# Optimization experiments

Hardware: AMD Instinct MI355X
Metric: run time of the kernel (lower is better)

Reference implementation:

```python
import jax, jax.numpy as jnp
import numpy as np

DIM = 384
HEADS = 12
K = 3          # kernel_size
PAD = 1
STRIDE = 1
B, H, W = 8, 56, 56


def conv1x1(x, w, b=None):
    # x: [B,C,H,W], w: [O,C]
    y = jnp.einsum('bchw,oc->bohw', x, w)
    if b is not None:
        y = y + b[None, :, None, None]
    return y


def unfold(x, k, p, s):
    # torch nn.Unfold: returns patches [B, C, k*k, nH, nW], kernel row-major, channel-major overall
    Bx, C, Hx, Wx = x.shape
    nH = (Hx + 2 * p - k) // s + 1
    nW = (Wx + 2 * p - k) // s + 1
    xp = jnp.pad(x, ((0, 0), (0, 0), (p, p), (p, p)))
    cols = [xp[:, :, i:i + s * nH:s, j:j + s * nW:s] for i in range(k) for j in range(k)]
    return jnp.stack(cols, axis=2), nH, nW


def fold(col, Hx, Wx, k, p, s):
    # torch F.fold (col2im): scatter-add overlapping windows. col: [B, C, k*k, nH, nW]
    Bx, C, _, nH, nW = col.shape
    canvas = jnp.zeros((Bx, C, Hx + 2 * p, Wx + 2 * p), col.dtype)
    idx = 0
    for i in range(k):
        for j in range(k):
            canvas = canvas.at[:, :, i:i + s * nH:s, j:j + s * nW:s].add(col[:, :, idx])
            idx += 1
    return canvas[:, :, p:p + Hx, p:p + Wx]


def setup_inputs() -> dict:
    key = jax.random.key(0)
    ks = jax.random.split(key, 5)
    k2 = K * K
    x = jax.random.normal(ks[0], (B, DIM, H, W), dtype=jnp.float32)
    v_w = jax.random.normal(ks[1], (DIM, DIM), dtype=jnp.float32) * 0.02
    v_b = jnp.zeros((DIM,), dtype=jnp.float32)
    attn_w = jax.random.normal(ks[2], (k2 * k2 * HEADS, DIM), dtype=jnp.float32) * 0.02
    proj_w = jax.random.normal(ks[3], (DIM, DIM), dtype=jnp.float32) * 0.02
    return {'x': x, 'v_w': v_w, 'v_b': v_b, 'attn_w': attn_w, 'proj_w': proj_w}


def reference(x, v_w, v_b, attn_w, proj_w):
    Bx, C, Hx, Wx = x.shape
    k2 = K * K
    hd = C // HEADS  # head dim
    # value projection + unfold into overlapping k x k windows
    v = conv1x1(x, v_w, v_b)
    vcol, nH, nW = unfold(v, K, PAD, STRIDE)        # [B, C, k2, nH, nW]
    L = nH * nW
    v = vcol.reshape(Bx, HEADS, hd, k2, L)          # split C = (heads, hd), heads slow
    v = v.transpose(0, 1, 4, 3, 2)                  # [B, n, L, k2(d), hd]
    # adaptive avg pool to (nH, nW); with stride=1 this is identity (pool window 1)
    ph, pw = Hx // nH, Wx // nW
    xp = x.reshape(Bx, C, nH, ph, nW, pw).mean(axis=(3, 5))
    # per-pixel attention logits, channel layout = ((i*k2 + d)*HEADS + head)
    a = jnp.einsum('bchw,oc->bohw', xp, attn_w)     # [B, k2*k2*n, nH, nW]
    a = a.reshape(Bx, k2, k2, HEADS, L)             # [B, i, d, n, L]
    a = a.transpose(0, 3, 4, 1, 2)                  # [B, n, L, i, d]
    a = jax.nn.softmax(a, axis=-1)
    out = jnp.einsum('bnlid,bnldh->bnlih', a, v)    # [B, n, L, i, hd]
    out = out.transpose(0, 1, 4, 3, 2)              # [B, n, hd, i, L] -> channel (n*hd+h)
    out = out.reshape(Bx, C, k2, nH, nW)
    out = fold(out, Hx, Wx, K, PAD, STRIDE)         # scatter-add windows back
    return conv1x1(out, proj_w)
```

## Files before the change

### kernel.cpp

```cpp
#include <hip/hip_runtime.h>
#include <hip/hip_bf16.h>

#define DIM   384
#define HEADS 12
#define K2    9
#define HH    56
#define WW    56
#define HWP   3136
#define BB    8
#define AO    972
#define AOP   976
#define MCAT  1408
#define PP    3200
#define PPAD  3600
#define W60   60

#define WBLK     2688
#define HALOBLK  696

typedef __hip_bfloat16 bf16;
typedef short bf16x8 __attribute__((ext_vector_type(8)));
typedef short bf16x4v __attribute__((ext_vector_type(4)));
typedef float f32x4 __attribute__((ext_vector_type(4)));
typedef float f32x2 __attribute__((ext_vector_type(2)));

static __device__ __forceinline__ float b2f(bf16 v) { return __bfloat162float(v); }
static __device__ __forceinline__ float bs2f(short s) {
    return __uint_as_float(((unsigned int)(unsigned short)s) << 16);
}
static __device__ __forceinline__ short f2bs(float f) {
    __hip_bfloat16 h = __float2bfloat16(f);
    return *(short*)&h;
}
static __device__ __forceinline__ f32x2 unpk(unsigned int u) {
    f32x2 r;
    r[0] = __uint_as_float(u << 16);
    r[1] = __uint_as_float(u & 0xffff0000u);
    return r;
}

static __device__ __forceinline__ void gl_lds16(const bf16* g, bf16* l) {
    __builtin_amdgcn_global_load_lds(
        (const __attribute__((address_space(1))) unsigned int*)g,
        (__attribute__((address_space(3))) unsigned int*)l, 16, 0, 0);
}

__global__ __launch_bounds__(256) void prep_kernel(
        const float* __restrict__ x, const float* __restrict__ v_w,
        const float* __restrict__ attn_w, const float* __restrict__ proj_w,
        bf16* __restrict__ xT, bf16* __restrict__ wcat, bf16* __restrict__ wp,
        bf16* __restrict__ vP) {
    const int bid = blockIdx.x;
    if (bid < 400) {
        const int lane = threadIdx.x & 63, w = threadIdx.x >> 6;
        const int p = (bid % 50) * 64 + lane;
        const int b = bid / 50;
        bf16* dst = xT + ((size_t)b * PP + p) * DIM;
        if (p >= HWP) {
            bf16x8 z = {};
            for (int cg = w; cg < 48; cg += 4) *(bf16x8*)(dst + cg * 8) = z;
            return;
        }
        const float* src = x + (size_t)b * DIM * HWP + p;
        for (int cg = w; cg < 48; cg += 4) {
            bf16x8 v;
#pragma unroll
            for (int j = 0; j < 8; j++) v[j] = f2bs(src[(size_t)(cg * 8 + j) * HWP]);
            *(bf16x8*)(dst + cg * 8) = v;
        }
    } else if (bid < 400 + WBLK) {
        const int idx = (bid - 400) * 256 + threadIdx.x;
        const int NCAT = MCAT * DIM;
        if (idx < NCAT) {
            const int row = idx / DIM, col = idx % DIM;
            float v;
            if (row < 384) v = v_w[row * DIM + col];
            else { const int r2 = row - 384; v = (r2 < AO) ? attn_w[r2 * DIM + col] : 0.f; }
            *(short*)&wcat[idx] = f2bs(v);
        } else {
            const int j = idx - NCAT;
            if (j < 384 * DIM) *(short*)&wp[j] = f2bs(proj_w[j]);
        }
    } else {
        const int hidx = (bid - 400 - WBLK) * 256 + threadIdx.x;
        const int b = hidx / 22272;
        const int r = hidx % 22272;
        const int hp = r / 48, cgi = r % 48;
        int row, col;
        if (hp < 240) {
            const int rr = hp / 60;
            row = (rr < 2) ? rr : rr + 56;
            col = hp % 60;
        } else {
            const int h2 = hp - 240;
            row = 2 + (h2 >> 2);
            const int c4 = h2 & 3;
            col = (c4 < 2) ? c4 : c4 + 56;
        }
        bf16x8 z = {};
        *(bf16x8*)(vP + ((size_t)b * PPAD + row * W60 + col) * DIM + cgi * 8) = z;
    }
}

#define GEMM_STAGE(Ab, Bb, lA, lB, koff)                                       \
    {                                                                          \
        _Pragma("unroll")                                                      \
        for (int r = 0; r < 4; r++) {                                          \
            int idx = r * 256 + t;                                             \
            int row = idx >> 3;                                                \
            int kq = ((idx & 7) - (row >> 1)) & 7;                             \
            gl_lds16(Ab + (size_t)row * DIM + (koff) + kq * 8, lA + idx * 8);  \
        }                                                                      \
        _Pragma("unroll")                                                      \
        for (int r = 0; r < 4; r++) {                                          \
            int idx = r * 256 + t;                                             \
            int row = idx >> 3;                                                \
            int kq = ((idx & 7) - (row >> 1)) & 7;                             \
            gl_lds16(Bb + (size_t)row * DIM + (koff) + kq * 8, lB + idx * 8);  \
        }                                                                      \
    }

#define GEMM_COMPUTE(lA, lB, acc)                                              \
    __builtin_amdgcn_s_setprio(1);                                             \
    _Pragma("unroll")                                                          \
    for (int h = 0; h < 2; h++) {                                              \
        const int swzh = (((h << 2) + quad + (l16 >> 1)) & 7) * 8;             \
        bf16x8 af[4], bfr[4];                                                  \
        _Pragma("unroll")                                                      \
        for (int mt = 0; mt < 4; mt++)                                         \
            af[mt] = *(const bf16x8*)((lA) + (wm * 64 + mt * 16 + l16) * 64 + swzh); \
        _Pragma("unroll")                                                      \
        for (int nt = 0; nt < 4; nt++)                                         \
            bfr[nt] = *(const bf16x8*)((lB) + (wn * 64 + nt * 16 + l16) * 64 + swzh); \
        _Pragma("unroll")                                                      \
        for (int mt = 0; mt < 4; mt++)                                         \
            _Pragma("unroll")                                                  \
            for (int nt = 0; nt < 4; nt++)                                     \
                acc[mt][nt] = __builtin_amdgcn_mfma_f32_16x16x32_bf16(         \
                    af[mt], bfr[nt], acc[mt][nt], 0, 0, 0);                    \
    }                                                                          \
    __builtin_amdgcn_s_setprio(0);

#define GEMM_KSTEP(cA, cB, sA, sB, koff)                                       \
    GEMM_STAGE(Ab, Bb, sA, sB, koff)                                           \
    asm volatile("s_waitcnt vmcnt(8)" ::: "memory");                           \
    __builtin_amdgcn_s_barrier();                                              \
    GEMM_COMPUTE(cA, cB, acc)                                                  \
    asm volatile("s_waitcnt lgkmcnt(0)" ::: "memory");                         \
    __builtin_amdgcn_s_barrier();

#define GEMM_MAIN_LOOP_V6(Ab, Bb, acc)                                         \
    GEMM_STAGE(Ab, Bb, lA0, lB0, 0)                                            \
    GEMM_KSTEP(lA0, lB0, lA1, lB1, 64)                                         \
    GEMM_KSTEP(lA1, lB1, lA0, lB0, 128)                                        \
    GEMM_KSTEP(lA0, lB0, lA1, lB1, 192)                                        \
    GEMM_KSTEP(lA1, lB1, lA0, lB0, 256)                                        \
    GEMM_KSTEP(lA0, lB0, lA1, lB1, 320)                                        \
    asm volatile("s_waitcnt vmcnt(0)" ::: "memory");                           \
    __builtin_amdgcn_s_barrier();                                              \
    GEMM_COMPUTE(lA1, lB1, acc)

__global__ __launch_bounds__(256) void gemm12_kernel(
        const bf16* __restrict__ A, const bf16* __restrict__ Bt,
        const float* __restrict__ bias, bf16* __restrict__ vP,
        bf16* __restrict__ lT) {
    __shared__ bf16 lds[32768];
    bf16* lA0 = lds;
    bf16* lB0 = lds + 8192;
    bf16* lA1 = lds + 16384;
    bf16* lB1 = lds + 24576;
    const int t = threadIdx.x;
    const int lane = t & 63, w = t >> 6;
    const int wm = w & 1, wn = w >> 1;
    const int quad = lane >> 4, l16 = lane & 15;

    const int bid = blockIdx.x;
    const int swz = (bid & 7) * 275 + (bid >> 3);
    const int mtile = swz % 11;
    const int nb = swz / 11;
    const int ntile = nb % 25;
    const int b = nb / 25;
    const int n0 = ntile * 128;
    const int m0 = mtile * 128;

    const bf16* Ab = A + (size_t)m0 * DIM;
    const bf16* Bb = Bt + ((size_t)b * PP + n0) * DIM;

    f32x4 acc[4][4] = {};
    GEMM_MAIN_LOOP_V6(Ab, Bb, acc)

    const bool isv = (m0 < 384);
    const int ch0 = isv ? m0 : m0 - 384;

    bf16* wbuf = lds + w * 1152;
    const int nr = lane >> 2;
    const int mc = (lane & 3) * 16;
#pragma unroll
    for (int nt = 0; nt < 4; nt++) {
#pragma unroll
        for (int mt = 0; mt < 4; mt++) {
            float4 bi = make_float4(0.f, 0.f, 0.f, 0.f);
            if (isv) bi = *(const float4*)(bias + ch0 + wm * 64 + mt * 16 + quad * 4);
            bf16x4v pk;
            pk[0] = f2bs(acc[mt][nt][0] + bi.x);
            pk[1] = f2bs(acc[mt][nt][1] + bi.y);
            pk[2] = f2bs(acc[mt][nt][2] + bi.z);
            pk[3] = f2bs(acc[mt][nt][3] + bi.w);
            *(bf16x4v*)(wbuf + l16 * 72 + mt * 16 + quad * 4) = pk;
        }
        bf16x8 v0 = *(const bf16x8*)(wbuf + nr * 72 + mc);
        bf16x8 v1 = *(const bf16x8*)(wbuf + nr * 72 + mc + 8);
        const int p = n0 + wn * 64 + nt * 16 + nr;
        const int cc = ch0 + wm * 64 + mc;
        if (p < HWP && (isv || cc < AOP)) {
            bf16* dp;
            if (isv) {
                const int y = p / WW;
                dp = vP + ((size_t)b * PPAD + p + y * 4 + 122) * DIM + cc;
            } else {
                dp = lT + ((size_t)b * PP + p) * AOP + cc;
            }
            *(bf16x8*)dp = v0;
            *(bf16x8*)(dp + 8) = v1;
        }
    }
}

__global__ __launch_bounds__(256) void gemm_planar_kernel(
        const bf16* __restrict__ A, const bf16* __restrict__ Bt,
        float* __restrict__ out) {
    __shared__ bf16 lds[32768];
    bf16* lA0 = lds;
    bf16* lB0 = lds + 8192;
    bf16* lA1 = lds + 16384;
    bf16* lB1 = lds + 24576;
    const int t = threadIdx.x;
    const int lane = t & 63, w = t >> 6;
    const int wm = w & 1, wn = w >> 1;
    const int quad = lane >> 4, l16 = lane & 15;

    const int bid = blockIdx.x;
    const int swz = (bid & 7) * 75 + (bid >> 3);
    const int mtile = swz % 3;
    const int nb = swz / 3;
    const int ntile = nb % 25;
    const int b = nb / 25;
    const int n0 = ntile * 128;
    const int m0 = mtile * 128;

    const bf16* Ab = A + (size_t)m0 * DIM;
    const bf16* Bb = Bt + ((size_t)b * PP + n0) * DIM;

    f32x4 acc[4][4] = {};
    GEMM_MAIN_LOOP_V6(Ab, Bb, acc)

#pragma unroll
    for (int mt = 0; mt < 4; mt++) {
#pragma unroll
        for (int nt = 0; nt < 4; nt++) {
            int p = n0 + wn * 64 + nt * 16 + l16;
            if (p >= HWP) continue;
#pragma unroll
            for (int reg = 0; reg < 4; reg++) {
                int o = m0 + wm * 64 + mt * 16 + quad * 4 + reg;
                out[((size_t)b * DIM + o) * HWP + p] = acc[mt][nt][reg];
            }
        }
    }
}

__global__ __launch_bounds__(384) void attn_fold_kernel(
        const bf16* __restrict__ lT, const bf16* __restrict__ vP,
        bf16* __restrict__ cT) {
    __shared__ bf16 P[8 * 9 * 12 * 9];
    __shared__ float Wf[8 * 25 * 12];
    const int t = threadIdx.x;
    const int b = blockIdx.x & 7;
    const int pix0 = (blockIdx.x >> 3) * 8;
    const int Y = pix0 / WW, X0 = pix0 % WW;

    for (int r = t; r < 864; r += 384) {
        const int px = r / 108, rem = r % 108;
        const int i = rem / 12, n = rem % 12;
        const int ir = i / 3, ic = i % 3;
        const int yi = Y + 1 - ir, xi = X0 + px + 1 - ic;
        bf16* Pd = &P[r * 9];
        if (yi < 0 || yi >= HH || xi < 0 || xi >= WW) {
#pragma unroll
            for (int d = 0; d < K2; d++) *(short*)&Pd[d] = 0;
        } else {
            const bf16* base = lT + ((size_t)b * PP + yi * WW + xi) * AOP + i * 108 + n;
            float lv[K2];
            float m = -1e30f;
#pragma unroll
            for (int d = 0; d < K2; d++) {
                lv[d] = b2f(base[d * 12]);
                m = fmaxf(m, lv[d]);
            }
            float s = 0.f;
#pragma unroll
            for (int d = 0; d < K2; d++) { lv[d] = __expf(lv[d] - m); s += lv[d]; }
            const float inv = 1.f / s;
#pragma unroll
            for (int d = 0; d < K2; d++) *(short*)&Pd[d] = f2bs(lv[d] * inv);
        }
    }
    __syncthreads();

    if (t < 300) {
        const int off = t / 12, n = t % 12;
        const int dy = off / 5 - 2, dx = off % 5 - 2;
        const int ir_lo = max(0, -dy), ir_hi = min(2, 2 - dy);
        const int ic_lo = max(0, -dx), ic_hi = min(2, 2 - dx);
#pragma unroll
        for (int px = 0; px < 8; px++) {
            float wsum = 0.f;
            for (int ir = ir_lo; ir <= ir_hi; ir++)
                for (int ic = ic_lo; ic <= ic_hi; ic++) {
                    const int i = ir * 3 + ic;
                    const int d = (dy + ir) * 3 + (dx + ic);
                    wsum += b2f(P[((px * 9 + i) * 12 + n) * 9 + d]);
                }
            Wf[(px * 25 + off) * 12 + n] = wsum;
        }
    }
    __syncthreads();

    const int px = t / 48, cg = t % 48;
    const int X = X0 + px;
    const int n = cg >> 2;
    const float* Wp = &Wf[px * 300 + n];
    const bf16* vbp = vP + ((size_t)b * PPAD + (size_t)(Y + 2) * W60 + (X + 2)) * DIM + cg * 8;
    f32x2 a2[4] = {};
#pragma unroll
    for (int dy = -2; dy <= 2; dy++) {
        const bf16* rowb = vbp + dy * (W60 * DIM);
        const float* wrow = Wp + (dy + 2) * 60;
#pragma unroll
        for (int dx = -2; dx <= 2; dx++) {
            const float w = wrow[(dx + 2) * 12];
            const uint4 d = *(const uint4*)(rowb + dx * DIM);
            f32x2 w2; w2[0] = w; w2[1] = w;
            a2[0] = __builtin_elementwise_fma(unpk(d.x), w2, a2[0]);
            a2[1] = __builtin_elementwise_fma(unpk(d.y), w2, a2[1]);
            a2[2] = __builtin_elementwise_fma(unpk(d.z), w2, a2[2]);
            a2[3] = __builtin_elementwise_fma(unpk(d.w), w2, a2[3]);
        }
    }
    bf16x8 po;
#pragma unroll
    for (int j = 0; j < 4; j++) {
        po[2 * j]     = f2bs(a2[j][0]);
        po[2 * j + 1] = f2bs(a2[j][1]);
    }
    *(bf16x8*)(cT + ((size_t)b * PP + pix0 + px) * DIM + cg * 8) = po;
}

extern "C" void kernel_launch(void* const* d_in, const int* in_sizes, int n_in,
                              void* d_out, int out_size, void* d_ws, size_t ws_size,
                              hipStream_t stream) {
    const float* x      = (const float*)d_in[0];
    const float* v_w    = (const float*)d_in[1];
    const float* v_b    = (const float*)d_in[2];
    const float* attn_w = (const float*)d_in[3];
    const float* proj_w = (const float*)d_in[4];
    float* out = (float*)d_out;

    bf16* xT    = (bf16*)d_ws;
    bf16* vP    = xT + (size_t)BB * PP * DIM;
    bf16* lT    = vP + (size_t)BB * PPAD * DIM;
    bf16* wcat  = lT + (size_t)BB * PP * AOP;
    bf16* wp    = wcat + (size_t)MCAT * DIM;
    bf16* cT    = xT;

    const int nprep = 400 + WBLK + HALOBLK;
    prep_kernel<<<nprep, 256, 0, stream>>>(x, v_w, attn_w, proj_w, xT, wcat, wp, vP);

    gemm12_kernel<<<2200, 256, 0, stream>>>(wcat, xT, v_b, vP, lT);
    attn_fold_kernel<<<3136, 384, 0, stream>>>(lT, vP, cT);
    gemm_planar_kernel<<<600, 256, 0, stream>>>(wp, cT, out);
}
```

Baseline: 202.8 us.

## Keep B tile resident in LDS and loop over all M tiles per block

The fused value/logit GEMM now loads a 64-column slice of the activation matrix (full K=384) into LDS once per block. It then iterates over all 11 weight row-tiles, streaming A in double-buffered 64-wide K chunks. This removes repeated re-reads of the activation tile across M tiles and cuts the grid from 2200 to 400 blocks. The cost is larger LDS use, a smaller per-wave N tile, and fewer blocks to cover the GPU's 256 CUs.

```diff
diff --git a/kernel.cpp b/kernel.cpp
--- a/kernel.cpp
+++ b/kernel.cpp
@@ -160,68 +160,132 @@
     __builtin_amdgcn_s_barrier();                                              \
     GEMM_COMPUTE(lA1, lB1, acc)
 
+#define STAGE_A7(mi, kg, dst)                                                  \
+    { _Pragma("unroll")                                                        \
+      for (int r = 0; r < 4; r++) {                                            \
+          int idx = r * 256 + t;                                               \
+          int row = idx >> 3;                                                  \
+          int kq = ((idx & 7) - (row >> 1)) & 7;                               \
+          gl_lds16(A + (size_t)((mi) * 128 + row) * DIM + (kg) * 64 + kq * 8,  \
+                   dst + idx * 8);                                             \
+      } }
+
+#define COMPUTE7(lA, kg, acc)                                                  \
+    __builtin_amdgcn_s_setprio(1);                                             \
+    _Pragma("unroll")                                                          \
+    for (int h = 0; h < 2; h++) {                                              \
+        const int swzh = (((h << 2) + quad + (l16 >> 1)) & 7) * 8;             \
+        bf16x8 af[4], bfr[2];                                                  \
+        _Pragma("unroll")                                                      \
+        for (int mt = 0; mt < 4; mt++)                                         \
+            af[mt] = *(const bf16x8*)((lA) + (wm * 64 + mt * 16 + l16) * 64 + swzh); \
+        _Pragma("unroll")                                                      \
+        for (int nt = 0; nt < 2; nt++)                                         \
+            bfr[nt] = *(const bf16x8*)(lBres + (wn * 32 + nt * 16 + l16) * 384 + (kg) * 64 + swzh); \
+        _Pragma("unroll")                                                      \
+        for (int mt = 0; mt < 4; mt++)                                         \
+            _Pragma("unroll")                                                  \
+            for (int nt = 0; nt < 2; nt++)                                     \
+                acc[mt][nt] = __builtin_amdgcn_mfma_f32_16x16x32_bf16(         \
+                    af[mt], bfr[nt], acc[mt][nt], 0, 0, 0);                    \
+    }                                                                          \
+    __builtin_amdgcn_s_setprio(0);
+
+#define KSTEP7(curA, kg, stage, vm)                                            \
+    stage                                                                      \
+    asm volatile("s_waitcnt vmcnt(" #vm ")" ::: "memory");                     \
+    __builtin_amdgcn_s_barrier();                                              \
+    COMPUTE7(curA, kg, acc)                                                    \
+    asm volatile("s_waitcnt lgkmcnt(0)" ::: "memory");                         \
+    __builtin_amdgcn_s_barrier();
+
 __global__ __launch_bounds__(256) void gemm12_kernel(
         const bf16* __restrict__ A, const bf16* __restrict__ Bt,
         const float* __restrict__ bias, bf16* __restrict__ vP,
         bf16* __restrict__ lT) {
-    __shared__ bf16 lds[32768];
-    bf16* lA0 = lds;
-    bf16* lB0 = lds + 8192;
-    bf16* lA1 = lds + 16384;
-    bf16* lB1 = lds + 24576;
+    __shared__ bf16 lds[40960];
+    bf16* lBres = lds;
+    bf16* lA0 = lds + 24576;
+    bf16* lA1 = lds + 32768;
     const int t = threadIdx.x;
     const int lane = t & 63, w = t >> 6;
     const int wm = w & 1, wn = w >> 1;
     const int quad = lane >> 4, l16 = lane & 15;
 
     const int bid = blockIdx.x;
-    const int swz = (bid & 7) * 275 + (bid >> 3);
-    const int mtile = swz % 11;
-    const int nb = swz / 11;
-    const int ntile = nb % 25;
-    const int b = nb / 25;
-    const int n0 = ntile * 128;
-    const int m0 = mtile * 128;
-
-    const bf16* Ab = A + (size_t)m0 * DIM;
+    const int b = bid & 7;
+    const int n0 = (bid >> 3) * 64;
+
     const bf16* Bb = Bt + ((size_t)b * PP + n0) * DIM;
 
-    f32x4 acc[4][4] = {};
-    GEMM_MAIN_LOOP_V6(Ab, Bb, acc)
-
-    const bool isv = (m0 < 384);
-    const int ch0 = isv ? m0 : m0 - 384;
-
-    bf16* wbuf = lds + w * 1152;
+    #pragma unroll
+    for (int r = 0; r < 12; r++) {
+        int idx = r * 256 + t;
+        int row = idx / 48;
+        int oct = idx % 48;
+        int g = oct >> 3, o = oct & 7;
+        int kq = (o - (row >> 1)) & 7;
+        gl_lds16(Bb + (size_t)row * DIM + g * 64 + kq * 8, lBres + idx * 8);
+    }
+    STAGE_A7(0, 0, lA0)
+
     const int nr = lane >> 2;
     const int mc = (lane & 3) * 16;
-#pragma unroll
-    for (int nt = 0; nt < 4; nt++) {
-#pragma unroll
-        for (int mt = 0; mt < 4; mt++) {
-            float4 bi = make_float4(0.f, 0.f, 0.f, 0.f);
-            if (isv) bi = *(const float4*)(bias + ch0 + wm * 64 + mt * 16 + quad * 4);
-            bf16x4v pk;
-            pk[0] = f2bs(acc[mt][nt][0] + bi.x);
-            pk[1] = f2bs(acc[mt][nt][1] + bi.y);
-            pk[2] = f2bs(acc[mt][nt][2] + bi.z);
-            pk[3] = f2bs(acc[mt][nt][3] + bi.w);
-            *(bf16x4v*)(wbuf + l16 * 72 + mt * 16 + quad * 4) = pk;
-        }
-        bf16x8 v0 = *(const bf16x8*)(wbuf + nr * 72 + mc);
-        bf16x8 v1 = *(const bf16x8*)(wbuf + nr * 72 + mc + 8);
-        const int p = n0 + wn * 64 + nt * 16 + nr;
-        const int cc = ch0 + wm * 64 + mc;
-        if (p < HWP && (isv || cc < AOP)) {
-            bf16* dp;
-            if (isv) {
-                const int y = p / WW;
-                dp = vP + ((size_t)b * PPAD + p + y * 4 + 122) * DIM + cc;
-            } else {
-                dp = lT + ((size_t)b * PP + p) * AOP + cc;
+
+    for (int mi = 0; mi < 11; mi++) {
+        f32x4 acc[4][2];
+        #pragma unroll
+        for (int mt = 0; mt < 4; mt++)
+            #pragma unroll
+            for (int nt = 0; nt < 2; nt++) acc[mt][nt] = (f32x4){0.f, 0.f, 0.f, 0.f};
+
+        KSTEP7(lA0, 0, STAGE_A7(mi, 1, lA1), 4)
+        KSTEP7(lA1, 1, STAGE_A7(mi, 2, lA0), 4)
+        KSTEP7(lA0, 2, STAGE_A7(mi, 3, lA1), 4)
+        KSTEP7(lA1, 3, STAGE_A7(mi, 4, lA0), 4)
+        KSTEP7(lA0, 4, STAGE_A7(mi, 5, lA1), 4)
+        if (mi < 10) {
+            KSTEP7(lA1, 5, STAGE_A7(mi + 1, 0, lA0), 4)
+        } else {
+            KSTEP7(lA1, 5, , 0)
+        }
+
+        const int m0 = mi * 128;
+        const bool isv = (mi < 3);
+        const int ch0 = isv ? m0 : m0 - 384;
+        bf16* wbuf = lA1 + w * 1152;
+        #pragma unroll
+        for (int nt = 0; nt < 2; nt++) {
+            #pragma unroll
+            for (int mt = 0; mt < 4; mt++) {
+                float4 bi = make_float4(0.f, 0.f, 0.f, 0.f);
+                if (isv) bi = *(const float4*)(bias + ch0 + wm * 64 + mt * 16 + quad * 4);
+                bf16x4v pk;
+                pk[0] = f2bs(acc[mt][nt][0] + bi.x);
+                pk[1] = f2bs(acc[mt][nt][1] + bi.y);
+                pk[2] = f2bs(acc[mt][nt][2] + bi.z);
+                pk[3] = f2bs(acc[mt][nt][3] + bi.w);
+                *(bf16x4v*)(wbuf + l16 * 72 + mt * 16 + quad * 4) = pk;
             }
-            *(bf16x8*)dp = v0;
-            *(bf16x8*)(dp + 8) = v1;
+            bf16x8 v0 = *(const bf16x8*)(wbuf + nr * 72 + mc);
+            bf16x8 v1 = *(const bf16x8*)(wbuf + nr * 72 + mc + 8);
+            const int p = n0 + wn * 32 + nt * 16 + nr;
+            const int cc = ch0 + wm * 64 + mc;
+            if (p < HWP && (isv || cc < AOP)) {
+                bf16* dp;
+                if (isv) {
+                    const int y = p / WW;
+                    dp = vP + ((size_t)b * PPAD + p + y * 4 + 122) * DIM + cc;
+                } else {
+                    dp = lT + ((size_t)b * PP + p) * AOP + cc;
+                }
+                *(bf16x8*)dp = v0;
+                *(bf16x8*)(dp + 8) = v1;
+            }
+        }
+        if (mi < 10) {
+            asm volatile("s_waitcnt lgkmcnt(0)" ::: "memory");
+            __builtin_amdgcn_s_barrier();
         }
     }
 }
@@ -376,7 +440,7 @@
     const int nprep = 400 + WBLK + HALOBLK;
     prep_kernel<<<nprep, 256, 0, stream>>>(x, v_w, attn_w, proj_w, xT, wcat, wp, vP);
 
-    gemm12_kernel<<<2200, 256, 0, stream>>>(wcat, xT, v_b, vP, lT);
+    gemm12_kernel<<<400, 256, 0, stream>>>(wcat, xT, v_b, vP, lT);
     attn_fold_kernel<<<3136, 384, 0, stream>>>(lT, vP, cT);
     gemm_planar_kernel<<<600, 256, 0, stream>>>(wp, cT, out);
 }
```

New measurement: 209.8 us. 3.4% more time.
